# Optimization experiments

Hardware: AMD Instinct MI355X
Metric: run time of the kernel (lower is better)

The kernel has to match this reference:

```python
import jax, jax.numpy as jnp
import numpy as np

IN_NC, OUT_NC, K = 64, 64, 3          # adc_in_nc, adc_out_nc, adc_kers
FC_SIZE = 512
FMN0, FMN1 = 512, 512
GROUP_FC = 4
CNN_PARA = IN_NC * OUT_NC * K * K + OUT_NC  # 36928
B, H, W = 16, 128, 128


def setup_inputs() -> dict:
    key = jax.random.key(0)
    ks = jax.random.split(key, 8)
    s = 0.05
    return {
        "x": jax.random.normal(ks[0], (B, IN_NC, H, W), jnp.float32),
        "fc_in": jax.random.normal(ks[1], (B, FC_SIZE), jnp.float32),
        "w1": jax.random.normal(ks[2], (FMN0, FC_SIZE), jnp.float32) * s,
        "b1": jax.random.normal(ks[3], (FMN0,), jnp.float32) * s,
        "w2": jax.random.normal(ks[4], (FMN1, FMN0), jnp.float32) * s,
        "b2": jax.random.normal(ks[5], (FMN1,), jnp.float32) * s,
        # grouped 1x1 conv1d: [groups, out_per_group, in_per_group]
        "w3": jax.random.normal(ks[6], (GROUP_FC, CNN_PARA // GROUP_FC, FMN1 // GROUP_FC), jnp.float32) * s,
        "b3": jax.random.normal(ks[7], (CNN_PARA,), jnp.float32) * s,
        "splits": B,
    }


def _fmn(fc_in, w1, b1, w2, b2, w3, b3):
    # per-sample MLP (Conv1d with kernel 1 over length-1 sequence)
    h = jax.nn.relu(fc_in @ w1.T + b1)                      # [B, FMN0]
    h = jax.nn.relu(h @ w2.T + b2)                          # [B, FMN1]
    hg = h.reshape(h.shape[0], GROUP_FC, -1)                # [B, G, FMN1/G]
    o = jnp.einsum('bgi,goi->bgo', hg, w3)                  # [B, G, CNN_PARA/G]
    o = o.reshape(h.shape[0], -1) + b3                      # [B, CNN_PARA]
    return jax.nn.relu(o)


def reference(x, fc_in, w1, b1, w2, b2, w3, b3, splits):
    batch, C, Hx, Wx = x.shape
    wb = _fmn(fc_in, w1, b1, w2, b2, w3, b3)                # [B, CNN_PARA]
    weight = wb[:, :-OUT_NC].reshape(splits * OUT_NC, IN_NC, K, K)
    bias = wb[:, -OUT_NC:].reshape(-1)                      # [B*OUT_NC]
    # per-sample conv via grouped conv (groups = batch), VALID padding, stride 1
    y = jax.lax.conv_general_dilated(
        x.reshape(1, batch * C, Hx, Wx), weight,
        window_strides=(1, 1), padding='VALID',
        feature_group_count=batch,
        dimension_numbers=('NCHW', 'OIHW', 'NCHW'))          # [1, B*OUT, H', W']
    y = y + bias[None, :, None, None]
    # match torch conv3d output shape [1, B*OUT, 1, H', W']
    return y.reshape(1, batch * OUT_NC, 1, y.shape[-2], y.shape[-1])
```

## Files before the change

### kernel.cpp

```cpp
#include <hip/hip_runtime.h>
#include <hip/hip_bf16.h>

constexpr int BATCH   = 16;
constexpr int IN_NC   = 64;
constexpr int OUT_NC  = 64;
constexpr int KS      = 3;
constexpr int FC      = 512;
constexpr int GROUPS  = 4;
constexpr int CNN_PARA = IN_NC * OUT_NC * KS * KS + OUT_NC;
constexpr int PER_G   = CNN_PARA / GROUPS;
constexpr int IN_PER_G = FC / GROUPS;
constexpr int H = 128, W = 128;
constexpr int HO = 126, WO = 126;
constexpr int PIX = HO * WO;
constexpr int WCOUNT = IN_NC * OUT_NC * KS * KS;
constexpr int HW = H * W;

typedef __attribute__((ext_vector_type(8))) short short8;
typedef __attribute__((ext_vector_type(4))) float f32x4;

static __device__ __forceinline__ short bf16_bits(float f) {
    union { __hip_bfloat16 h; short s; } u;
    u.h = __float2bfloat16(f);
    return u.s;
}

__global__ __launch_bounds__(256) void mlp_layer(
    const float* __restrict__ in,
    const float* __restrict__ w,
    const float* __restrict__ bias,
    float* __restrict__ out)
{
    __shared__ float hs[BATCH * FC];
    int tid = threadIdx.x;
    for (int i = tid; i < BATCH * FC; i += 256) hs[i] = in[i];
    __syncthreads();

    int o = blockIdx.x * 4 + (tid >> 6);
    int l = tid & 63;
    const float4* wrow = (const float4*)(w + (size_t)o * FC + l * 8);
    float4 w0 = wrow[0], w1 = wrow[1];

    float acc[BATCH];
#pragma unroll
    for (int b = 0; b < BATCH; ++b) {
        const float4* hp = (const float4*)(hs + b * FC + l * 8);
        float4 h0 = hp[0], h1 = hp[1];
        acc[b] = w0.x * h0.x + w0.y * h0.y + w0.z * h0.z + w0.w * h0.w
               + w1.x * h1.x + w1.y * h1.y + w1.z * h1.z + w1.w * h1.w;
    }
#pragma unroll
    for (int off = 32; off > 0; off >>= 1)
#pragma unroll
        for (int b = 0; b < BATCH; ++b)
            acc[b] += __shfl_down(acc[b], off, 64);
    if (l == 0) {
        float bv = bias[o];
#pragma unroll
        for (int b = 0; b < BATCH; ++b) {
            float v = acc[b] + bv;
            out[b * FC + o] = v > 0.f ? v : 0.f;
        }
    }
}

__global__ __launch_bounds__(256) void grouped_fc(
    const float* __restrict__ h2,
    const float* __restrict__ w3,
    const float* __restrict__ b3,
    float* __restrict__ wb)
{
    __shared__ float hs[BATCH * FC];
    int tid = threadIdx.x;
    for (int i = tid; i < BATCH * FC; i += 256) hs[i] = h2[i];
    __syncthreads();

    int j = blockIdx.x * 4 + (tid >> 6);
    int l = tid & 63;
    int g = j / PER_G;
    const float2 wv = *(const float2*)(w3 + (size_t)j * IN_PER_G + l * 2);
    const float* hbase = hs + g * IN_PER_G + l * 2;

    float acc[BATCH];
#pragma unroll
    for (int b = 0; b < BATCH; ++b)
        acc[b] = wv.x * hbase[b * FC] + wv.y * hbase[b * FC + 1];
#pragma unroll
    for (int off = 32; off > 0; off >>= 1)
#pragma unroll
        for (int b = 0; b < BATCH; ++b)
            acc[b] += __shfl_down(acc[b], off, 64);
    if (l == 0) {
        float bv = b3[j];
#pragma unroll
        for (int b = 0; b < BATCH; ++b) {
            float v = acc[b] + bv;
            wb[(size_t)b * CNN_PARA + j] = v > 0.f ? v : 0.f;
        }
    }
}

__global__ __launch_bounds__(256) void conv_w_transpose(
    const float* __restrict__ wb, __hip_bfloat16* __restrict__ wT)
{
    int idx = blockIdx.x * blockDim.x + threadIdx.x;
    if (idx >= BATCH * 9 * 4096) return;
    int b    = idx / (9 * 4096);
    int r    = idx % (9 * 4096);
    int kykx = r >> 12;
    int q    = r & 4095;
    int oc   = q >> 6;
    int ic   = q & 63;
    float v = wb[(size_t)b * CNN_PARA + (oc * 64 + ic) * 9 + kykx];
    union { __hip_bfloat16 h; short s; } u; u.s = bf16_bits(v);
    wT[idx] = u.h;
}

__global__ __launch_bounds__(256) void conv_x_transpose(
    const float* __restrict__ x, __hip_bfloat16* __restrict__ xT)
{
    __shared__ float lds[64][129];
    int blk = blockIdx.x;
    int b = blk >> 7, h = blk & 127;
    int tid = threadIdx.x;

    const float* xrow = x + (size_t)b * IN_NC * HW + (size_t)h * W;
#pragma unroll 8
    for (int it = 0; it < 32; ++it) {
        int ic = it * 2 + (tid >> 7);
        int w  = tid & 127;
        lds[ic][w] = xrow[(size_t)ic * HW + w];
    }
    __syncthreads();

    __hip_bfloat16* dst = xT + ((size_t)(b * 128 + h)) * (128 * 64);
#pragma unroll
    for (int i = 0; i < 4; ++i) {
        int chunk = i * 256 + tid;
        int w = chunk >> 3, oct = chunk & 7;
        short8 v;
#pragma unroll
        for (int j = 0; j < 8; ++j) v[j] = bf16_bits(lds[oct * 8 + j][w]);
        *(short8*)(dst + (size_t)w * 64 + oct * 8) = v;
    }
}

__global__ __launch_bounds__(256, 4) void conv_mfma(
    const __hip_bfloat16* __restrict__ xT,
    const __hip_bfloat16* __restrict__ wT,
    const float* __restrict__ wb,
    float* __restrict__ out)
{
    int wg   = blockIdx.x;
    int sblk = (wg & 7) * 126 + (wg >> 3);
    int b    = sblk / 63;
    int rp   = sblk % 63;

    int tid = threadIdx.x;
    int wv = tid >> 6, l = tid & 63;
    int l15 = l & 15, l4 = l >> 4;
    int row = rp * 2 + (wv >> 1);
    int px0 = (wv & 1) * 64;

    f32x4 acc[4][4];
#pragma unroll
    for (int mf = 0; mf < 4; ++mf)
#pragma unroll
        for (int nf = 0; nf < 4; ++nf) acc[mf][nf] = (f32x4)0.f;

#pragma unroll
    for (int kykx = 0; kykx < 9; ++kykx) {
        int ky = kykx / 3, kx = kykx % 3;
        const __hip_bfloat16* wtile = wT + (size_t)(b * 9 + kykx) * 4096;
        const __hip_bfloat16* xrow =
            xT + ((size_t)(b * 128 + row + ky) * 128 + kx) * 64;
#pragma unroll
        for (int ks = 0; ks < 2; ++ks) {
            int ic0 = ks * 32 + l4 * 8;
            short8 A[4];
#pragma unroll
            for (int mf = 0; mf < 4; ++mf)
                A[mf] = *(const short8*)(wtile + (mf * 16 + l15) * 64 + ic0);
#pragma unroll
            for (int nf = 0; nf < 4; ++nf) {
                int ox = px0 + nf * 16 + l15;
                short8 bf = *(const short8*)(xrow + (size_t)ox * 64 + ic0);
#pragma unroll
                for (int mf = 0; mf < 4; ++mf)
                    acc[mf][nf] = __builtin_amdgcn_mfma_f32_16x16x32_bf16(
                        A[mf], bf, acc[mf][nf], 0, 0, 0);
            }
        }
    }

    float bias[4][4];
#pragma unroll
    for (int mf = 0; mf < 4; ++mf)
#pragma unroll
        for (int r = 0; r < 4; ++r)
            bias[mf][r] = wb[(size_t)b * CNN_PARA + WCOUNT + mf * 16 + l4 * 4 + r];

#pragma unroll
    for (int mf = 0; mf < 4; ++mf)
#pragma unroll
        for (int nf = 0; nf < 4; ++nf) {
            int ox = px0 + nf * 16 + l15;
            if (ox >= WO) continue;
#pragma unroll
            for (int r = 0; r < 4; ++r) {
                int oc = mf * 16 + l4 * 4 + r;
                out[((size_t)(b * 64 + oc)) * PIX + row * WO + ox]
                    = acc[mf][nf][r] + bias[mf][r];
            }
        }
}

__global__ __launch_bounds__(256) void conv_direct(
    const float* __restrict__ x, const float* __restrict__ wb,
    float* __restrict__ out)
{
    constexpr int NBLK = (PIX + 255) / 256;
    __shared__ float wsm[IN_NC * 9];
    __shared__ float bias_s;
    int bid  = blockIdx.x;
    int tile = bid % NBLK;
    int boc  = bid / NBLK;
    int b = boc >> 6, oc = boc & 63;
    int tid = threadIdx.x;
    const float* wsrc = wb + (size_t)b * CNN_PARA + oc * (IN_NC * 9);
    if (tid < IN_NC * 9 / 4) ((float4*)wsm)[tid] = ((const float4*)wsrc)[tid];
    if (tid == 0) bias_s = wb[(size_t)b * CNN_PARA + WCOUNT + oc];
    __syncthreads();
    int p = tile * 256 + tid;
    if (p >= PIX) return;
    int oy = p / WO, ox = p - oy * WO;
    const float* xb = x + (size_t)b * IN_NC * HW + oy * W + ox;
    float acc = bias_s;
    for (int ic = 0; ic < IN_NC; ++ic) {
        const float* xr = xb + ic * HW;
        const float* wr = wsm + ic * 9;
#pragma unroll
        for (int ky = 0; ky < 3; ++ky) {
            acc += xr[ky * W + 0] * wr[ky * 3 + 0];
            acc += xr[ky * W + 1] * wr[ky * 3 + 1];
            acc += xr[ky * W + 2] * wr[ky * 3 + 2];
        }
    }
    out[(size_t)boc * PIX + p] = acc;
}

extern "C" void kernel_launch(void* const* d_in, const int* in_sizes, int n_in,
                              void* d_out, int out_size, void* d_ws, size_t ws_size,
                              hipStream_t stream) {
    const float* x     = (const float*)d_in[0];
    const float* fc_in = (const float*)d_in[1];
    const float* w1    = (const float*)d_in[2];
    const float* b1    = (const float*)d_in[3];
    const float* w2    = (const float*)d_in[4];
    const float* b2    = (const float*)d_in[5];
    const float* w3    = (const float*)d_in[6];
    const float* b3    = (const float*)d_in[7];
    float* out = (float*)d_out;

    const size_t off_h1 = 0;
    const size_t off_h2 = off_h1 + (size_t)BATCH * FC * 4;
    const size_t off_wb = off_h2 + (size_t)BATCH * FC * 4;
    const size_t off_wT = off_wb + (size_t)BATCH * CNN_PARA * 4;
    const size_t off_xT = off_wT + (size_t)BATCH * 9 * 4096 * 2;
    const size_t xT_bytes = (size_t)BATCH * 128 * 128 * 64 * 2 + 16384;
    const size_t need = off_xT + xT_bytes;

    float* h1 = (float*)((char*)d_ws + off_h1);
    float* h2 = (float*)((char*)d_ws + off_h2);
    float* wb = (float*)((char*)d_ws + off_wb);

    mlp_layer<<<FC / 4, 256, 0, stream>>>(fc_in, w1, b1, h1);
    mlp_layer<<<FC / 4, 256, 0, stream>>>(h1, w2, b2, h2);
    grouped_fc<<<CNN_PARA / 4, 256, 0, stream>>>(h2, w3, b3, wb);

    if (ws_size >= need) {
        __hip_bfloat16* wT = (__hip_bfloat16*)((char*)d_ws + off_wT);
        __hip_bfloat16* xT = (__hip_bfloat16*)((char*)d_ws + off_xT);
        conv_w_transpose<<<(BATCH * 9 * 4096 + 255) / 256, 256, 0, stream>>>(wb, wT);
        conv_x_transpose<<<BATCH * 128, 256, 0, stream>>>(x, xT);
        conv_mfma<<<BATCH * 63, 256, 0, stream>>>(xT, wT, wb, out);
    } else {
        conv_direct<<<BATCH * OUT_NC * ((PIX + 255) / 256), 256, 0, stream>>>(x, wb, out);
    }
}
```

Measured before the change: 280.0 us.

## Stage input rows in swizzled LDS for conv MFMA and tile weight transpose

The conv MFMA kernel now copies the four input rows each workgroup needs into shared memory, using an XOR swizzle to avoid bank conflicts. The nine kernel taps then read from LDS instead of re-reading the same pixels from global memory for every tap. The weight transpose kernel is rewritten to stage each 8-output-channel block in LDS and write 16-byte vectors. In exchange, about 67KB of LDS per block lowers occupancy (launch bounds go from 4 to 2) and adds a barrier before compute.

```diff
diff --git a/kernel.cpp b/kernel.cpp
--- a/kernel.cpp
+++ b/kernel.cpp
@@ -103,17 +103,26 @@
 __global__ __launch_bounds__(256) void conv_w_transpose(
     const float* __restrict__ wb, __hip_bfloat16* __restrict__ wT)
 {
-    int idx = blockIdx.x * blockDim.x + threadIdx.x;
-    if (idx >= BATCH * 9 * 4096) return;
-    int b    = idx / (9 * 4096);
-    int r    = idx % (9 * 4096);
-    int kykx = r >> 12;
-    int q    = r & 4095;
-    int oc   = q >> 6;
-    int ic   = q & 63;
-    float v = wb[(size_t)b * CNN_PARA + (oc * 64 + ic) * 9 + kykx];
-    union { __hip_bfloat16 h; short s; } u; u.s = bf16_bits(v);
-    wT[idx] = u.h;
+    __shared__ float wsm[8 * 576];
+    int blk = blockIdx.x;
+    int b = blk >> 3, ocg = blk & 7;
+    int tid = threadIdx.x;
+    const float* src = wb + (size_t)b * CNN_PARA + ocg * 8 * 576;
+    for (int i = tid; i < 8 * 576; i += 256) wsm[i] = src[i];
+    __syncthreads();
+
+    for (int c = tid; c < 576; c += 256) {
+        int kykx  = c / 64;
+        int r     = c & 63;
+        int oc_l  = r >> 3;
+        int icoct = r & 7;
+        short8 v;
+#pragma unroll
+        for (int j = 0; j < 8; ++j)
+            v[j] = bf16_bits(wsm[oc_l * 576 + (icoct * 8 + j) * 9 + kykx]);
+        *(short8*)(wT + (size_t)b * 9 * 4096 + kykx * 4096
+                   + (ocg * 8 + oc_l) * 64 + icoct * 8) = v;
+    }
 }
 
 __global__ __launch_bounds__(256) void conv_x_transpose(
@@ -145,12 +154,19 @@
     }
 }
 
-__global__ __launch_bounds__(256, 4) void conv_mfma(
+constexpr int SLAB_PX    = 132;
+constexpr int SLAB_BYTES = SLAB_PX * 64 * 2;
+constexpr int XS_BYTES   = 4 * SLAB_BYTES;
+constexpr int NCHUNK     = XS_BYTES / 16;
+
+__global__ __launch_bounds__(256, 2) void conv_mfma(
     const __hip_bfloat16* __restrict__ xT,
     const __hip_bfloat16* __restrict__ wT,
     const float* __restrict__ wb,
     float* __restrict__ out)
 {
+    __shared__ __align__(16) char xs[XS_BYTES];
+
     int wg   = blockIdx.x;
     int sblk = (wg & 7) * 126 + (wg >> 3);
     int b    = sblk / 63;
@@ -159,8 +175,29 @@
     int tid = threadIdx.x;
     int wv = tid >> 6, l = tid & 63;
     int l15 = l & 15, l4 = l >> 4;
+
+    {
+        const char* xbase = (const char*)xT;
+#pragma unroll
+        for (int i = 0; i < (NCHUNK + 255) / 256; ++i) {
+            int c = tid + i * 256;
+            if (c < NCHUNK) {
+                int D   = c * 16;
+                int r   = D / SLAB_BYTES;
+                int rem = D - r * SLAB_BYTES;
+                int p   = rem >> 7;
+                int c16 = D & 127;
+                short8 v = *(const short8*)(xbase
+                    + (size_t)(b * 128 + rp * 2 + r) * 16384 + (size_t)(p * 128 + c16));
+                *(short8*)(xs + r * SLAB_BYTES + p * 128 + (c16 ^ ((p & 7) << 4))) = v;
+            }
+        }
+    }
+    __syncthreads();
+
     int row = rp * 2 + (wv >> 1);
     int px0 = (wv & 1) * 64;
+    int lr  = wv >> 1;
 
     f32x4 acc[4][4];
 #pragma unroll
@@ -172,23 +209,25 @@
     for (int kykx = 0; kykx < 9; ++kykx) {
         int ky = kykx / 3, kx = kykx % 3;
         const __hip_bfloat16* wtile = wT + (size_t)(b * 9 + kykx) * 4096;
-        const __hip_bfloat16* xrow =
-            xT + ((size_t)(b * 128 + row + ky) * 128 + kx) * 64;
+        const char* xslab = xs + (lr + ky) * SLAB_BYTES;
+        int pxk = kx + px0;
+        int sw  = ((kx + l15) & 7) << 4;
 #pragma unroll
         for (int ks = 0; ks < 2; ++ks) {
-            int ic0 = ks * 32 + l4 * 8;
+            int ic0  = ks * 32 + l4 * 8;
+            int slot = ((ks * 4 + l4) * 16) ^ sw;
             short8 A[4];
 #pragma unroll
             for (int mf = 0; mf < 4; ++mf)
                 A[mf] = *(const short8*)(wtile + (mf * 16 + l15) * 64 + ic0);
 #pragma unroll
             for (int nf = 0; nf < 4; ++nf) {
-                int ox = px0 + nf * 16 + l15;
-                short8 bf = *(const short8*)(xrow + (size_t)ox * 64 + ic0);
+                int p = pxk + nf * 16 + l15;
+                short8 bfr = *(const short8*)(xslab + p * 128 + slot);
 #pragma unroll
                 for (int mf = 0; mf < 4; ++mf)
                     acc[mf][nf] = __builtin_amdgcn_mfma_f32_16x16x32_bf16(
-                        A[mf], bf, acc[mf][nf], 0, 0, 0);
+                        A[mf], bfr, acc[mf][nf], 0, 0, 0);
             }
         }
     }
@@ -281,7 +320,7 @@
     if (ws_size >= need) {
         __hip_bfloat16* wT = (__hip_bfloat16*)((char*)d_ws + off_wT);
         __hip_bfloat16* xT = (__hip_bfloat16*)((char*)d_ws + off_xT);
-        conv_w_transpose<<<(BATCH * 9 * 4096 + 255) / 256, 256, 0, stream>>>(wb, wT);
+        conv_w_transpose<<<BATCH * 8, 256, 0, stream>>>(wb, wT);
         conv_x_transpose<<<BATCH * 128, 256, 0, stream>>>(x, xT);
         conv_mfma<<<BATCH * 63, 256, 0, stream>>>(xT, wT, wb, out);
     } else {
```

Result: faster. 251.7 us (-10.1%).
